# Performance work log

Measured on AMD Instinct MI355X. Metric: run time of the kernel, lower is better.

## Reference

```python
import jax, jax.numpy as jnp
import numpy as np

B, R, CIN, J, O, ITERS = 512, 1152, 8, 10, 16, 3  # batch, routes, in_ch, capsules, out_ch, routing iters


def squash(s, axis):
    # v = (||s||^2 / (1 + ||s||^2)) * s / ||s||  (standard CapsNet squash)
    sq = jnp.sum(s * s, axis=axis, keepdims=True)
    return (sq / (1.0 + sq)) * s * jax.lax.rsqrt(sq + 1e-8)


def setup_inputs() -> dict:
    key = jax.random.key(0)
    k1, k2 = jax.random.split(key)
    x = jax.random.normal(k1, (B, R, CIN), dtype=jnp.float32)
    W = jax.random.normal(k2, (R, J, O, CIN), dtype=jnp.float32)  # param, batch-broadcast
    return {"x": x, "W": W}


def reference(x, W):
    # u_hat[b,r,j,:] = W[r,j] @ x[b,r]   (replaces torch stack/cat broadcasting)
    u_hat = jnp.einsum('rjoc,brc->brjo', W, x)  # [B,R,J,O]
    b_ij = jnp.zeros((x.shape[0], R, J), dtype=x.dtype)
    v = None
    for it in range(ITERS):
        c_ij = jax.nn.softmax(b_ij, axis=2)                 # softmax over capsules j
        s_j = jnp.einsum('brj,brjo->bjo', c_ij, u_hat)      # weighted sum over routes
        v = squash(s_j, axis=-1)                            # [B,J,O]
        if it < ITERS - 1:
            b_ij = b_ij + jnp.einsum('brjo,bjo->brj', u_hat, v)  # agreement
    # torch returns v_j.squeeze(1) with shape [B, J, O, 1]
    return v[..., None]
```

## Files before the change

kernel.cpp:

```cpp
#include <hip/hip_runtime.h>
#include <hip/hip_bf16.h>
#include <cstdint>
#include <cstddef>

#define NB 512
#define NR 1152
#define NC 8
#define NJ 10
#define NO 16
#define NJO 160

typedef unsigned int uint32;

__device__ __forceinline__ uint32 f2bf(float f) {
    uint32 x = __float_as_uint(f);
    return (x + 0x7fffu + ((x >> 16) & 1u)) >> 16;
}
__device__ __forceinline__ float bflo(uint32 w) { return __uint_as_float(w << 16); }
__device__ __forceinline__ float bfhi(uint32 w) { return __uint_as_float(w & 0xffff0000u); }

#define UVAL(k) (((k) & 1) ? bfhi(u32[(k) >> 1]) : bflo(u32[(k) >> 1]))

__global__ __launch_bounds__(320) void uhat_kernel(const float* __restrict__ x,
                                                   const float* __restrict__ W,
                                                   uint32* __restrict__ u ) {
    const int r = blockIdx.x;
    const int t = threadIdx.x;

    __shared__ float Ws[NC][NJO];
    __shared__ float xs[NB][NC];

    for (int i = t; i < NJO * NC; i += 320) {
        Ws[i & 7][i >> 3] = W[(size_t)r * (NJO * NC) + i];
    }
    for (int i = t; i < NB * NC; i += 320) {
        int b = i >> 3, c = i & 7;
        xs[b][c] = x[(size_t)b * (NR * NC) + r * NC + c];
    }
    __syncthreads();

    const int jo2  = t % 80;
    const int half = t / 80;

    float w0[8], w1[8];
#pragma unroll
    for (int c = 0; c < 8; ++c) {
        w0[c] = Ws[c][2 * jo2];
        w1[c] = Ws[c][2 * jo2 + 1];
    }

    for (int b = half; b < NB; b += 4) {
        const float4* xp = (const float4*)xs[b];
        float4 xa = xp[0], xb = xp[1];
        float a0 = w0[0] * xa.x + w0[1] * xa.y + w0[2] * xa.z + w0[3] * xa.w
                 + w0[4] * xb.x + w0[5] * xb.y + w0[6] * xb.z + w0[7] * xb.w;
        float a1 = w1[0] * xa.x + w1[1] * xa.y + w1[2] * xa.z + w1[3] * xa.w
                 + w1[4] * xb.x + w1[5] * xb.y + w1[6] * xb.z + w1[7] * xb.w;
        uint32 p = f2bf(a0) | (f2bf(a1) << 16);
        u[(size_t)(b * NR + r) * 80 + jo2] = p;
    }
}

template <bool UNIFORM>
__global__ __launch_bounds__(64) void pass_kernel(const uint32* __restrict__ u,
                                                  const float* __restrict__ vsum,
                                                  float* __restrict__ s) {
    const int b    = blockIdx.y;
    const int lane = threadIdx.x;
    const int r    = blockIdx.x * 64 + lane;

    __shared__ float vs[NJO];
    if (!UNIFORM) {
        for (int i = lane; i < NJO; i += 64) vs[i] = vsum[b * NJO + i];
        __syncthreads();
    }

    uint32 u32[80];
    const uint4* up = (const uint4*)(u + (size_t)(b * NR + r) * 80);
#pragma unroll
    for (int i = 0; i < 20; ++i) {
        uint4 q = up[i];
        u32[4 * i + 0] = q.x;
        u32[4 * i + 1] = q.y;
        u32[4 * i + 2] = q.z;
        u32[4 * i + 3] = q.w;
    }

    float cj[NJ];
    if (UNIFORM) {
#pragma unroll
        for (int j = 0; j < NJ; ++j) cj[j] = 1.0f / NJ;
    } else {
        float bj[NJ];
        const float4* vp = (const float4*)vs;
#pragma unroll
        for (int j = 0; j < NJ; ++j) {
            float acc = 0.0f;
#pragma unroll
            for (int q = 0; q < 4; ++q) {
                float4 v4 = vp[j * 4 + q];
                acc += v4.x * UVAL(j * 16 + q * 4 + 0);
                acc += v4.y * UVAL(j * 16 + q * 4 + 1);
                acc += v4.z * UVAL(j * 16 + q * 4 + 2);
                acc += v4.w * UVAL(j * 16 + q * 4 + 3);
            }
            bj[j] = acc;
        }
        float m = bj[0];
#pragma unroll
        for (int j = 1; j < NJ; ++j) m = fmaxf(m, bj[j]);
        float sum = 0.0f;
#pragma unroll
        for (int j = 0; j < NJ; ++j) {
            float e = __expf(bj[j] - m);
            cj[j] = e;
            sum += e;
        }
        float inv = 1.0f / sum;
#pragma unroll
        for (int j = 0; j < NJ; ++j) cj[j] *= inv;
    }

    auto contrib = [&](int k) -> float {
        if (k >= NJO) return 0.0f;
        return cj[k >> 4] * UVAL(k);
    };

    float a[96];
    {
        const int bit = lane & 1;
#pragma unroll
        for (int i = 0; i < 96; ++i) {
            float lo = contrib(i);
            float hi = contrib(i + 96);
            float send = bit ? lo : hi;
            float recv = __shfl_xor(send, 1);
            a[i] = (bit ? hi : lo) + recv;
        }
    }
#pragma unroll
    for (int st = 1; st < 6; ++st) {
        const int h = 96 >> st;
        const int bit = (lane >> st) & 1;
#pragma unroll
        for (int i = 0; i < 48; ++i) {
            if (i < h) {
                float send = bit ? a[i] : a[i + h];
                float recv = __shfl_xor(send, 1 << st);
                a[i] = (bit ? a[i + h] : a[i]) + recv;
            }
        }
    }

    const int base = 3 * (__brev((uint32)lane) >> 26);
#pragma unroll
    for (int i = 0; i < 3; ++i) {
        int jo = base + i;
        if (jo < NJO) atomicAdd(&s[b * NJO + jo], a[i]);
    }
}

template <bool FINAL>
__global__ __launch_bounds__(256) void squash_kernel(const float* __restrict__ s,
                                                     float* __restrict__ vacc) {
    const int idx = blockIdx.x * 256 + threadIdx.x;
    float val = s[idx];
    float sq = val * val;
#pragma unroll
    for (int off = 1; off < 16; off <<= 1) sq += __shfl_xor(sq, off, 16);
    float scale = (sq / (1.0f + sq)) * rsqrtf(sq + 1e-8f);
    float v = val * scale;
    if (FINAL) vacc[idx] = v;
    else       vacc[idx] += v;
}

extern "C" void kernel_launch(void* const* d_in, const int* in_sizes, int n_in,
                              void* d_out, int out_size, void* d_ws, size_t ws_size,
                              hipStream_t stream) {
    (void)in_sizes; (void)n_in; (void)out_size; (void)ws_size;

    const float* x = (const float*)d_in[0];
    const float* W = (const float*)d_in[1];
    float* out = (float*)d_out;

    char* ws = (char*)d_ws;
    const size_t UBYTES = (size_t)NB * NR * NJO * 2;
    uint32* u   = (uint32*)ws;
    float* s0   = (float*)(ws + UBYTES);
    float* s1   = s0 + NB * NJO;
    float* s2   = s1 + NB * NJO;
    float* vsum = s2 + NB * NJO;

    hipMemsetAsync(s0, 0, (size_t)4 * NB * NJO * sizeof(float), stream);

    uhat_kernel<<<NR, 320, 0, stream>>>(x, W, u);

    pass_kernel<true><<<dim3(NR / 64, NB), 64, 0, stream>>>(u, nullptr, s0);
    squash_kernel<false><<<(NB * NJO) / 256, 256, 0, stream>>>(s0, vsum);

    pass_kernel<false><<<dim3(NR / 64, NB), 64, 0, stream>>>(u, vsum, s1);
    squash_kernel<false><<<(NB * NJO) / 256, 256, 0, stream>>>(s1, vsum);

    pass_kernel<false><<<dim3(NR / 64, NB), 64, 0, stream>>>(u, vsum, s2);
    squash_kernel<true><<<(NB * NJO) / 256, 256, 0, stream>>>(s2, out);
}
```

Baseline: 265.3 us.

## Pre-transpose x for coalesced uhat loads and widen pass kernel blocks

After: 299.6 us. 12.9% more time.

```diff
diff --git a/kernel.cpp b/kernel.cpp
--- a/kernel.cpp
+++ b/kernel.cpp
@@ -21,7 +21,27 @@
 
 #define UVAL(k) (((k) & 1) ? bfhi(u32[(k) >> 1]) : bflo(u32[(k) >> 1]))
 
-__global__ __launch_bounds__(320) void uhat_kernel(const float* __restrict__ x,
+__global__ __launch_bounds__(256) void xpose_kernel(const float* __restrict__ x,
+                                                    float* __restrict__ xT) {
+    const int r0 = blockIdx.x * 16;
+    const int b0 = blockIdx.y * 64;
+    const int t  = threadIdx.x;
+    __shared__ float tile[16][65][8];
+
+    for (int i = t; i < 2048; i += 256) {
+        int b = i >> 5, r = (i >> 1) & 15, h = i & 1;
+        float4 v = *(const float4*)&x[(size_t)(b0 + b) * (NR * NC) + (size_t)(r0 + r) * NC + h * 4];
+        *(float4*)&tile[r][b][h * 4] = v;
+    }
+    __syncthreads();
+    for (int i = t; i < 2048; i += 256) {
+        int r = i >> 7, b = (i >> 1) & 63, h = i & 1;
+        float4 v = *(const float4*)&tile[r][b][h * 4];
+        *(float4*)&xT[(size_t)(r0 + r) * (NB * NC) + (size_t)(b0 + b) * NC + h * 4] = v;
+    }
+}
+
+__global__ __launch_bounds__(320) void uhat_kernel(const float* __restrict__ xT,
                                                    const float* __restrict__ W,
                                                    uint32* __restrict__ u ) {
     const int r = blockIdx.x;
@@ -33,9 +53,10 @@
     for (int i = t; i < NJO * NC; i += 320) {
         Ws[i & 7][i >> 3] = W[(size_t)r * (NJO * NC) + i];
     }
-    for (int i = t; i < NB * NC; i += 320) {
-        int b = i >> 3, c = i & 7;
-        xs[b][c] = x[(size_t)b * (NR * NC) + r * NC + c];
+    {
+        const float4* xsrc = (const float4*)(xT + (size_t)r * (NB * NC));
+        float4* xdst = (float4*)&xs[0][0];
+        for (int i = t; i < (NB * NC) / 4; i += 320) xdst[i] = xsrc[i];
     }
     __syncthreads();
 
@@ -62,16 +83,17 @@
 }
 
 template <bool UNIFORM>
-__global__ __launch_bounds__(64) void pass_kernel(const uint32* __restrict__ u,
-                                                  const float* __restrict__ vsum,
-                                                  float* __restrict__ s) {
+__global__ __launch_bounds__(384) void pass_kernel(const uint32* __restrict__ u,
+                                                   const float* __restrict__ vsum,
+                                                   float* __restrict__ s) {
     const int b    = blockIdx.y;
-    const int lane = threadIdx.x;
-    const int r    = blockIdx.x * 64 + lane;
+    const int t    = threadIdx.x;
+    const int lane = t & 63;
+    const int r    = blockIdx.x * 384 + t;
 
     __shared__ float vs[NJO];
     if (!UNIFORM) {
-        for (int i = lane; i < NJO; i += 64) vs[i] = vsum[b * NJO + i];
+        if (t < NJO) vs[t] = vsum[b * NJO + t];
         __syncthreads();
     }
 
@@ -184,23 +206,27 @@
     float* out = (float*)d_out;
 
     char* ws = (char*)d_ws;
+    const size_t XBYTES = (size_t)NR * NB * NC * 4;
     const size_t UBYTES = (size_t)NB * NR * NJO * 2;
-    uint32* u   = (uint32*)ws;
-    float* s0   = (float*)(ws + UBYTES);
+    float*  xT  = (float*)ws;
+    uint32* u   = (uint32*)(ws + XBYTES);
+    float* s0   = (float*)(ws + XBYTES + UBYTES);
     float* s1   = s0 + NB * NJO;
     float* s2   = s1 + NB * NJO;
     float* vsum = s2 + NB * NJO;
 
     hipMemsetAsync(s0, 0, (size_t)4 * NB * NJO * sizeof(float), stream);
 
-    uhat_kernel<<<NR, 320, 0, stream>>>(x, W, u);
-
-    pass_kernel<true><<<dim3(NR / 64, NB), 64, 0, stream>>>(u, nullptr, s0);
+    xpose_kernel<<<dim3(NR / 16, NB / 64), 256, 0, stream>>>(x, xT);
+
+    uhat_kernel<<<NR, 320, 0, stream>>>(xT, W, u);
+
+    pass_kernel<true><<<dim3(3, NB), 384, 0, stream>>>(u, nullptr, s0);
     squash_kernel<false><<<(NB * NJO) / 256, 256, 0, stream>>>(s0, vsum);
 
-    pass_kernel<false><<<dim3(NR / 64, NB), 64, 0, stream>>>(u, vsum, s1);
+    pass_kernel<false><<<dim3(3, NB), 384, 0, stream>>>(u, vsum, s1);
     squash_kernel<false><<<(NB * NJO) / 256, 256, 0, stream>>>(s1, vsum);
 
-    pass_kernel<false><<<dim3(NR / 64, NB), 64, 0, stream>>>(u, vsum, s2);
+    pass_kernel<false><<<dim3(3, NB), 384, 0, stream>>>(u, vsum, s2);
     squash_kernel<true><<<(NB * NJO) / 256, 256, 0, stream>>>(s2, out);
 }
```
